# Kernel optimization log

Hardware: AMD Instinct MI355X
Metric: run time of the kernel (lower is better)

Reference implementation:

```python
import jax, jax.numpy as jnp
import numpy as np

HEAD_SIZE = 64
N_EMBED = 1024
THETA = 10000.0


def _rope_cos_sin(T, dim):
    # freqs = 1/theta^(2i/dim), i in [0, dim//2)
    freqs = 1.0 / (THETA ** (jnp.arange(0, dim, 2, dtype=jnp.float32) / dim))  # (dim//2,)
    angles = jnp.arange(T, dtype=jnp.float32)[:, None] * freqs[None, :]        # (T, dim//2)
    return jnp.cos(angles), jnp.sin(angles)


def _apply_rope(q, cos, sin):
    # q: (B, T, hs); interpret consecutive pairs as complex (even=real, odd=imag)
    B, T, hs = q.shape
    qr = q.reshape(B, T, hs // 2, 2)
    ev, od = qr[..., 0], qr[..., 1]
    out_ev = ev * cos - od * sin
    out_od = ev * sin + od * cos
    return jnp.stack([out_ev, out_od], axis=-1).reshape(B, T, hs)


def setup_inputs() -> dict:
    key = jax.random.key(0)
    ks = jax.random.split(key, 7)
    B, T = 4, 2048
    s = 1.0 / np.sqrt(N_EMBED)
    return {
        "x": jax.random.normal(ks[0], (B, T, N_EMBED), dtype=jnp.float32),
        "mask": jnp.ones((B, T), dtype=jnp.int32),
        "Wq": jax.random.uniform(ks[1], (N_EMBED, HEAD_SIZE), jnp.float32, -s, s),
        "bq": jax.random.uniform(ks[2], (HEAD_SIZE,), jnp.float32, -s, s),
        "Wk": jax.random.uniform(ks[3], (N_EMBED, HEAD_SIZE), jnp.float32, -s, s),
        "bk": jax.random.uniform(ks[4], (HEAD_SIZE,), jnp.float32, -s, s),
        "Wv": jax.random.uniform(ks[5], (N_EMBED, HEAD_SIZE), jnp.float32, -s, s),
        "bv": jax.random.uniform(ks[6], (HEAD_SIZE,), jnp.float32, -s, s),
    }


def reference(x, mask, Wq, bq, Wk, bk, Wv, bv):
    B, T, C = x.shape
    Q = x @ Wq + bq  # (B, T, hs)
    K = x @ Wk + bk
    V = x @ Wv + bv

    cos, sin = _rope_cos_sin(T, HEAD_SIZE)
    Q = _apply_rope(Q, cos, sin)
    K = _apply_rope(K, cos, sin)

    causal = jnp.triu(jnp.ones((T, T), dtype=bool), k=1)[None, :, :]  # (1, T, T)
    pad = (mask == 0)[:, :, None]                                     # (B, T, 1) masks rows
    attn_mask = causal | pad                                          # (B, T, T)

    scores = jnp.einsum('btd,bsd->bts', Q, K) * (C ** -0.5)
    scores = jnp.where(attn_mask, -jnp.inf, scores)
    attn = jax.nn.softmax(scores, axis=-1)
    # dropout in eval mode: identity
    return jnp.einsum('bts,bsd->btd', attn, V)
```

## Files before the change

kernel.cpp:

```cpp
#include <hip/hip_runtime.h>
#include <math.h>


typedef __attribute__((ext_vector_type(8))) short short8v;
typedef __attribute__((ext_vector_type(4))) float f32x4;

__device__ __forceinline__ unsigned short f2bf(float f){
  unsigned int u = __float_as_uint(f);
  u += 0x7fffu + ((u >> 16) & 1u);
  return (unsigned short)(u >> 16);
}
__device__ __forceinline__ float bf2f(unsigned short h){
  return __uint_as_float(((unsigned int)h) << 16);
}
__device__ __forceinline__ f32x4 mfma16(short8v a, short8v b, f32x4 c){
  return __builtin_amdgcn_mfma_f32_16x16x32_bf16(a, b, c, 0, 0, 0);
}


__global__ __launch_bounds__(256) void prep_k(
    const float* __restrict__ Wq, const float* __restrict__ Wk, const float* __restrict__ Wv,
    unsigned short* __restrict__ WThi, unsigned short* __restrict__ WTlo,
    float2* __restrict__ rope)
{
  const int tid = blockIdx.x * 256 + threadIdx.x;
  #pragma unroll
  for (int it = 0; it < 3; ++it){
    const int idx = tid + 65536 * it;
    const int k = idx / 192;
    const int n = idx - k * 192;
    const float v = (n < 64) ? Wq[k*64 + n] : (n < 128 ? Wk[k*64 + n - 64] : Wv[k*64 + n - 128]);
    const unsigned short hi = f2bf(v);
    WThi[n*1024 + k] = hi;
    WTlo[n*1024 + k] = f2bf(v - bf2f(hi));
  }
  const int p = tid & 31, tt = tid >> 5;
  const float freq = exp2f((float)p * -0.4152410118609203f);
  float s, c;
  sincosf((float)tt * freq, &s, &c);
  rope[tid] = make_float2(c, s);
}

__global__ __launch_bounds__(256) void qkv_k(
    const float* __restrict__ x,
    const unsigned short* __restrict__ WThi, const unsigned short* __restrict__ WTlo,
    const float* __restrict__ bq, const float* __restrict__ bk, const float* __restrict__ bv,
    const float2* __restrict__ rope,
    unsigned short* __restrict__ Qhi, unsigned short* __restrict__ Qlo,
    unsigned short* __restrict__ Khi, unsigned short* __restrict__ Klo,
    unsigned short* __restrict__ VThi, unsigned short* __restrict__ VTlo)
{
  __shared__ __align__(16) unsigned short XAh[32][72], XAl[32][72];
  __shared__ __align__(16) unsigned short WTh[192][72], WTl[192][72];

  const int t = threadIdx.x;
  const int w = t >> 6, l = t & 63;
  const int h = w & 1, nh = w >> 1;
  const int g = l >> 4, c16 = l & 15;
  const int m0 = blockIdx.x * 32;

  f32x4 acc[6];
  #pragma unroll
  for (int nt = 0; nt < 6; ++nt) acc[nt] = (f32x4){0.f, 0.f, 0.f, 0.f};

  const int xr = t >> 3, xc = (t & 7) * 8;

  for (int k0 = 0; k0 < 1024; k0 += 64){
    __syncthreads();
    {
      const float* xp = &x[(m0 + xr) * 1024 + k0 + xc];
      const float4 a = *(const float4*)xp;
      const float4 b4 = *(const float4*)(xp + 4);
      const float f[8] = {a.x, a.y, a.z, a.w, b4.x, b4.y, b4.z, b4.w};
      union { short8v v; unsigned short u[8]; } hh, ll;
      #pragma unroll
      for (int j = 0; j < 8; ++j){
        hh.u[j] = f2bf(f[j]);
        ll.u[j] = f2bf(f[j] - bf2f(hh.u[j]));
      }
      *(short8v*)&XAh[xr][xc] = hh.v;
      *(short8v*)&XAl[xr][xc] = ll.v;
    }
    #pragma unroll
    for (int a = 0; a < 6; ++a){
      const int ch = t + 256 * a;
      const int wn = ch >> 3, wk = (ch & 7) * 8;
      *(short8v*)&WTh[wn][wk] = *(const short8v*)&WThi[wn*1024 + k0 + wk];
      *(short8v*)&WTl[wn][wk] = *(const short8v*)&WTlo[wn*1024 + k0 + wk];
    }
    __syncthreads();
    #pragma unroll
    for (int ks = 0; ks < 2; ++ks){
      const short8v ah = *(const short8v*)&XAh[16*h + c16][ks*32 + g*8];
      const short8v al2 = *(const short8v*)&XAl[16*h + c16][ks*32 + g*8];
      #pragma unroll
      for (int nt = 0; nt < 6; ++nt){
        const int wr = 96*nh + 16*nt + c16;
        const short8v bh = *(const short8v*)&WTh[wr][ks*32 + g*8];
        const short8v bl = *(const short8v*)&WTl[wr][ks*32 + g*8];
        acc[nt] = mfma16(ah, bh, acc[nt]);
        acc[nt] = mfma16(ah, bl, acc[nt]);
        acc[nt] = mfma16(al2, bh, acc[nt]);
      }
    }
  }

  #pragma unroll
  for (int nt = 0; nt < 6; ++nt){
    const int c = 96*nh + 16*nt + c16;
    const int m = c >> 6, cm = c & 63;
    const float* bptr = (m == 0) ? bq : (m == 1 ? bk : bv);
    const float bias = bptr[cm];
    #pragma unroll
    for (int i = 0; i < 4; ++i){
      const int gr = m0 + 16*h + 4*g + i;
      float v = acc[nt][i] + bias;
      const float other = __shfl_xor(v, 1);
      if (m < 2){
        const float2 cs = rope[(gr & 2047) * 32 + (cm >> 1)];
        v = (c & 1) ? fmaf(v, cs.x,  other * cs.y)
                    : fmaf(v, cs.x, -other * cs.y);
      }
      const unsigned short hi = f2bf(v);
      const unsigned short lo = f2bf(v - bf2f(hi));
      if (m == 0){ Qhi[gr*64 + cm] = hi; Qlo[gr*64 + cm] = lo; }
      else if (m == 1){ Khi[gr*64 + cm] = hi; Klo[gr*64 + cm] = lo; }
      else {
        const size_t a2 = ((size_t)(gr >> 11) * 64 + cm) * 2048 + (gr & 2047);
        VThi[a2] = hi; VTlo[a2] = lo;
      }
    }
  }
}

__global__ __launch_bounds__(256) void attn_k(
    const unsigned short* __restrict__ Qhi, const unsigned short* __restrict__ Qlo,
    const unsigned short* __restrict__ Khi, const unsigned short* __restrict__ Klo,
    const unsigned short* __restrict__ VThi, const unsigned short* __restrict__ VTlo,
    float* __restrict__ out)
{
  __shared__ __align__(16) unsigned short Kh[64][72], Kl[64][72];
  __shared__ __align__(16) unsigned short Vh[64][72], Vl[64][72];
  __shared__ __align__(16) unsigned short Ph[4][16][40], Pl[4][16][40];
  __shared__ float Om[2][16][68];
  __shared__ float Ml[2][16][2];

  const int t = threadIdx.x;
  const int w = t >> 6, l = t & 63;
  const int h = w & 1, kh = w >> 1;
  const int g = l >> 4, c16 = l & 15;
  const int b = blockIdx.y;
  const int q0 = (63 - (int)blockIdx.x) * 32;
  const size_t bT = (size_t)b * 2048;

  short8v qh[2], ql2[2];
  {
    const size_t qoff = (bT + q0 + 16*h + c16) * 64 + g*8;
    qh[0]  = *(const short8v*)&Qhi[qoff];
    qh[1]  = *(const short8v*)&Qhi[qoff + 32];
    ql2[0] = *(const short8v*)&Qlo[qoff];
    ql2[1] = *(const short8v*)&Qlo[qoff + 32];
  }

  f32x4 acc[4];
  #pragma unroll
  for (int nt = 0; nt < 4; ++nt) acc[nt] = (f32x4){0.f, 0.f, 0.f, 0.f};
  float m_run[4], l_run[4];
  #pragma unroll
  for (int i = 0; i < 4; ++i){ m_run[i] = -INFINITY; l_run[i] = 0.f; }

  const int sr = t >> 2, sc = (t & 3) * 16;
  const int nk = q0 / 64 + 1;

  for (int kt = 0; kt < nk; ++kt){
    const int k0 = kt * 64;
    __syncthreads();
    {
      const size_t koff = (bT + k0 + sr) * 64 + sc;
      *(short8v*)&Kh[sr][sc]     = *(const short8v*)&Khi[koff];
      *(short8v*)&Kh[sr][sc + 8] = *(const short8v*)&Khi[koff + 8];
      *(short8v*)&Kl[sr][sc]     = *(const short8v*)&Klo[koff];
      *(short8v*)&Kl[sr][sc + 8] = *(const short8v*)&Klo[koff + 8];
      const size_t voff = ((size_t)b * 64 + sr) * 2048 + k0 + sc;
      *(short8v*)&Vh[sr][sc]     = *(const short8v*)&VThi[voff];
      *(short8v*)&Vh[sr][sc + 8] = *(const short8v*)&VThi[voff + 8];
      *(short8v*)&Vl[sr][sc]     = *(const short8v*)&VTlo[voff];
      *(short8v*)&Vl[sr][sc + 8] = *(const short8v*)&VTlo[voff + 8];
    }
    __syncthreads();

    f32x4 s[2];
    #pragma unroll
    for (int t2 = 0; t2 < 2; ++t2){
      const int krow = 32*kh + 16*t2 + c16;
      const short8v bh0 = *(const short8v*)&Kh[krow][g*8];
      const short8v bl0 = *(const short8v*)&Kl[krow][g*8];
      const short8v bh1 = *(const short8v*)&Kh[krow][32 + g*8];
      const short8v bl1 = *(const short8v*)&Kl[krow][32 + g*8];
      f32x4 z = (f32x4){0.f, 0.f, 0.f, 0.f};
      z = mfma16(qh[0], bh0, z);
      z = mfma16(qh[0], bl0, z);
      z = mfma16(ql2[0], bh0, z);
      z = mfma16(qh[1], bh1, z);
      z = mfma16(qh[1], bl1, z);
      z = mfma16(ql2[1], bh1, z);
      s[t2] = z;
    }

    float sv[2][4];
    #pragma unroll
    for (int t2 = 0; t2 < 2; ++t2)
      #pragma unroll
      for (int i = 0; i < 4; ++i){
        float v = s[t2][i] * 0.03125f;
        if (kt == nk - 1){
          const int keyg = k0 + 32*kh + 16*t2 + c16;
          const int qg = q0 + 16*h + 4*g + i;
          if (keyg > qg) v = -INFINITY;
        }
        sv[t2][i] = v;
      }

    float al[4];
    #pragma unroll
    for (int i = 0; i < 4; ++i){
      float pm = fmaxf(sv[0][i], sv[1][i]);
      pm = fmaxf(pm, __shfl_xor(pm, 1));
      pm = fmaxf(pm, __shfl_xor(pm, 2));
      pm = fmaxf(pm, __shfl_xor(pm, 4));
      pm = fmaxf(pm, __shfl_xor(pm, 8));
      const float mnew = fmaxf(m_run[i], pm);
      const float msafe = fmaxf(mnew, -1e30f);
      al[i] = expf(m_run[i] - msafe);
      const float p0 = expf(sv[0][i] - msafe);
      const float p1 = expf(sv[1][i] - msafe);
      float ps = p0 + p1;
      ps += __shfl_xor(ps, 1);
      ps += __shfl_xor(ps, 2);
      ps += __shfl_xor(ps, 4);
      ps += __shfl_xor(ps, 8);
      l_run[i] = l_run[i] * al[i] + ps;
      m_run[i] = mnew;
      const unsigned short h0 = f2bf(p0);
      Ph[w][4*g + i][c16] = h0;
      Pl[w][4*g + i][c16] = f2bf(p0 - bf2f(h0));
      const unsigned short h1 = f2bf(p1);
      Ph[w][4*g + i][16 + c16] = h1;
      Pl[w][4*g + i][16 + c16] = f2bf(p1 - bf2f(h1));
    }

    #pragma unroll
    for (int nt = 0; nt < 4; ++nt)
      #pragma unroll
      for (int i = 0; i < 4; ++i) acc[nt][i] *= al[i];

    const short8v pah = *(const short8v*)&Ph[w][c16][g*8];
    const short8v pal = *(const short8v*)&Pl[w][c16][g*8];
    #pragma unroll
    for (int nt = 0; nt < 4; ++nt){
      const short8v vbh = *(const short8v*)&Vh[16*nt + c16][32*kh + g*8];
      const short8v vbl = *(const short8v*)&Vl[16*nt + c16][32*kh + g*8];
      acc[nt] = mfma16(pah, vbh, acc[nt]);
      acc[nt] = mfma16(pah, vbl, acc[nt]);
      acc[nt] = mfma16(pal, vbh, acc[nt]);
    }
  }

  if (kh == 1){
    #pragma unroll
    for (int nt = 0; nt < 4; ++nt)
      #pragma unroll
      for (int i = 0; i < 4; ++i)
        Om[h][4*g + i][16*nt + c16] = acc[nt][i];
    if (c16 == 0){
      #pragma unroll
      for (int i = 0; i < 4; ++i){
        Ml[h][4*g + i][0] = m_run[i];
        Ml[h][4*g + i][1] = l_run[i];
      }
    }
  }
  __syncthreads();
  if (kh == 0){
    float e0[4], e1[4], linv[4];
    #pragma unroll
    for (int i = 0; i < 4; ++i){
      const float mo  = Ml[h][4*g + i][0];
      const float lo2 = Ml[h][4*g + i][1];
      const float mm = fmaxf(m_run[i], mo);
      e0[i] = expf(m_run[i] - mm);
      e1[i] = (mo == -INFINITY) ? 0.f : expf(mo - mm);
      linv[i] = 1.f / (l_run[i] * e0[i] + lo2 * e1[i]);
    }
    #pragma unroll
    for (int nt = 0; nt < 4; ++nt)
      #pragma unroll
      for (int i = 0; i < 4; ++i){
        const float v = (acc[nt][i] * e0[i] + Om[h][4*g + i][16*nt + c16] * e1[i]) * linv[i];
        out[(bT + q0 + 16*h + 4*g + i) * 64 + 16*nt + c16] = v;
      }
  }
}

extern "C" void kernel_launch(void* const* d_in, const int* in_sizes, int n_in,
                              void* d_out, int out_size, void* d_ws, size_t ws_size,
                              hipStream_t stream) {
  (void)in_sizes; (void)n_in; (void)out_size; (void)ws_size;
  const float* x    = (const float*)d_in[0];
  const float* Wq   = (const float*)d_in[2];
  const float* bq   = (const float*)d_in[3];
  const float* Wk   = (const float*)d_in[4];
  const float* bk   = (const float*)d_in[5];
  const float* Wv   = (const float*)d_in[6];
  const float* bv   = (const float*)d_in[7];
  float* out = (float*)d_out;

  const size_t NROW = 8192;
  unsigned short* Qhi  = (unsigned short*)d_ws;
  unsigned short* Qlo  = Qhi  + NROW * 64;
  unsigned short* Khi  = Qlo  + NROW * 64;
  unsigned short* Klo  = Khi  + NROW * 64;
  unsigned short* VThi = Klo  + NROW * 64;
  unsigned short* VTlo = VThi + NROW * 64;
  unsigned short* WThi = VTlo + NROW * 64;
  unsigned short* WTlo = WThi + 192 * 1024;
  float2*         rope = (float2*)(WTlo + 192 * 1024);

  prep_k<<<dim3(256), dim3(256), 0, stream>>>(Wq, Wk, Wv, WThi, WTlo, rope);
  qkv_k<<<dim3(256), dim3(256), 0, stream>>>(x, WThi, WTlo, bq, bk, bv, rope,
                                             Qhi, Qlo, Khi, Klo, VThi, VTlo);
  attn_k<<<dim3(64, 4), dim3(256), 0, stream>>>(Qhi, Qlo, Khi, Klo, VThi, VTlo, out);
}
```

Baseline: 180.7 us.

## Drop split-bf16 Q/K/V in attention, use 512 threads and register prefetch

Q, K, V and P are now stored as a single bf16 value instead of a hi/lo split, so the attention MFMAs go from three per product to one. Both kernels move to 512 threads (8 waves), and attention splits each key tile across four wave groups whose partial softmax states are merged at the end. K/V for the next tile are prefetched into registers before the current tile is computed. Dropping the lo parts lowers accuracy, and the P·V MFMA zero-pads half its K dimension.

```diff
diff --git a/kernel.cpp b/kernel.cpp
--- a/kernel.cpp
+++ b/kernel.cpp
@@ -3,6 +3,7 @@
 
 
 typedef __attribute__((ext_vector_type(8))) short short8v;
+typedef __attribute__((ext_vector_type(4))) short short4v;
 typedef __attribute__((ext_vector_type(4))) float f32x4;
 
 __device__ __forceinline__ unsigned short f2bf(float f){
@@ -41,14 +42,13 @@
   rope[tid] = make_float2(c, s);
 }
 
-__global__ __launch_bounds__(256) void qkv_k(
+__global__ __launch_bounds__(512) void qkv_k(
     const float* __restrict__ x,
     const unsigned short* __restrict__ WThi, const unsigned short* __restrict__ WTlo,
     const float* __restrict__ bq, const float* __restrict__ bk, const float* __restrict__ bv,
     const float2* __restrict__ rope,
-    unsigned short* __restrict__ Qhi, unsigned short* __restrict__ Qlo,
-    unsigned short* __restrict__ Khi, unsigned short* __restrict__ Klo,
-    unsigned short* __restrict__ VThi, unsigned short* __restrict__ VTlo)
+    unsigned short* __restrict__ Qb, unsigned short* __restrict__ Kb,
+    unsigned short* __restrict__ VT)
 {
   __shared__ __align__(16) unsigned short XAh[32][72], XAl[32][72];
   __shared__ __align__(16) unsigned short WTh[192][72], WTl[192][72];
@@ -59,31 +59,29 @@
   const int g = l >> 4, c16 = l & 15;
   const int m0 = blockIdx.x * 32;
 
-  f32x4 acc[6];
-  #pragma unroll
-  for (int nt = 0; nt < 6; ++nt) acc[nt] = (f32x4){0.f, 0.f, 0.f, 0.f};
-
-  const int xr = t >> 3, xc = (t & 7) * 8;
+  f32x4 acc[3];
+  #pragma unroll
+  for (int nt = 0; nt < 3; ++nt) acc[nt] = (f32x4){0.f, 0.f, 0.f, 0.f};
+
+  const int xr = t >> 4, xc = (t & 15) * 4;
 
   for (int k0 = 0; k0 < 1024; k0 += 64){
     __syncthreads();
     {
-      const float* xp = &x[(m0 + xr) * 1024 + k0 + xc];
-      const float4 a = *(const float4*)xp;
-      const float4 b4 = *(const float4*)(xp + 4);
-      const float f[8] = {a.x, a.y, a.z, a.w, b4.x, b4.y, b4.z, b4.w};
-      union { short8v v; unsigned short u[8]; } hh, ll;
-      #pragma unroll
-      for (int j = 0; j < 8; ++j){
+      const float4 a4 = *(const float4*)&x[(m0 + xr) * 1024 + k0 + xc];
+      const float f[4] = {a4.x, a4.y, a4.z, a4.w};
+      union { short4v v; unsigned short u[4]; } hh, ll;
+      #pragma unroll
+      for (int j = 0; j < 4; ++j){
         hh.u[j] = f2bf(f[j]);
         ll.u[j] = f2bf(f[j] - bf2f(hh.u[j]));
       }
-      *(short8v*)&XAh[xr][xc] = hh.v;
-      *(short8v*)&XAl[xr][xc] = ll.v;
-    }
-    #pragma unroll
-    for (int a = 0; a < 6; ++a){
-      const int ch = t + 256 * a;
+      *(short4v*)&XAh[xr][xc] = hh.v;
+      *(short4v*)&XAl[xr][xc] = ll.v;
+    }
+    #pragma unroll
+    for (int a = 0; a < 3; ++a){
+      const int ch = t + 512 * a;
       const int wn = ch >> 3, wk = (ch & 7) * 8;
       *(short8v*)&WTh[wn][wk] = *(const short8v*)&WThi[wn*1024 + k0 + wk];
       *(short8v*)&WTl[wn][wk] = *(const short8v*)&WTlo[wn*1024 + k0 + wk];
@@ -91,11 +89,11 @@
     __syncthreads();
     #pragma unroll
     for (int ks = 0; ks < 2; ++ks){
-      const short8v ah = *(const short8v*)&XAh[16*h + c16][ks*32 + g*8];
+      const short8v ah  = *(const short8v*)&XAh[16*h + c16][ks*32 + g*8];
       const short8v al2 = *(const short8v*)&XAl[16*h + c16][ks*32 + g*8];
       #pragma unroll
-      for (int nt = 0; nt < 6; ++nt){
-        const int wr = 96*nh + 16*nt + c16;
+      for (int nt = 0; nt < 3; ++nt){
+        const int wr = 48*nh + 16*nt + c16;
         const short8v bh = *(const short8v*)&WTh[wr][ks*32 + g*8];
         const short8v bl = *(const short8v*)&WTl[wr][ks*32 + g*8];
         acc[nt] = mfma16(ah, bh, acc[nt]);
@@ -106,8 +104,8 @@
   }
 
   #pragma unroll
-  for (int nt = 0; nt < 6; ++nt){
-    const int c = 96*nh + 16*nt + c16;
+  for (int nt = 0; nt < 3; ++nt){
+    const int c = 48*nh + 16*nt + c16;
     const int m = c >> 6, cm = c & 63;
     const float* bptr = (m == 0) ? bq : (m == 1 ? bk : bv);
     const float bias = bptr[cm];
@@ -121,29 +119,22 @@
         v = (c & 1) ? fmaf(v, cs.x,  other * cs.y)
                     : fmaf(v, cs.x, -other * cs.y);
       }
-      const unsigned short hi = f2bf(v);
-      const unsigned short lo = f2bf(v - bf2f(hi));
-      if (m == 0){ Qhi[gr*64 + cm] = hi; Qlo[gr*64 + cm] = lo; }
-      else if (m == 1){ Khi[gr*64 + cm] = hi; Klo[gr*64 + cm] = lo; }
-      else {
-        const size_t a2 = ((size_t)(gr >> 11) * 64 + cm) * 2048 + (gr & 2047);
-        VThi[a2] = hi; VTlo[a2] = lo;
-      }
-    }
-  }
-}
-
-__global__ __launch_bounds__(256) void attn_k(
-    const unsigned short* __restrict__ Qhi, const unsigned short* __restrict__ Qlo,
-    const unsigned short* __restrict__ Khi, const unsigned short* __restrict__ Klo,
-    const unsigned short* __restrict__ VThi, const unsigned short* __restrict__ VTlo,
-    float* __restrict__ out)
+      if (m == 0)      Qb[gr*64 + cm] = f2bf(v);
+      else if (m == 1) Kb[gr*64 + cm] = f2bf(v);
+      else             VT[((size_t)(gr >> 11) * 64 + cm) * 2048 + (gr & 2047)] = f2bf(v);
+    }
+  }
+}
+
+__global__ __launch_bounds__(512) void attn_k(
+    const unsigned short* __restrict__ Qb, const unsigned short* __restrict__ Kb,
+    const unsigned short* __restrict__ VT, float* __restrict__ out)
 {
-  __shared__ __align__(16) unsigned short Kh[64][72], Kl[64][72];
-  __shared__ __align__(16) unsigned short Vh[64][72], Vl[64][72];
-  __shared__ __align__(16) unsigned short Ph[4][16][40], Pl[4][16][40];
-  __shared__ float Om[2][16][68];
-  __shared__ float Ml[2][16][2];
+  __shared__ __align__(16) unsigned short Kh[64][72];
+  __shared__ __align__(16) unsigned short Vh[64][72];
+  __shared__ __align__(16) unsigned short Ph[8][16][24];
+  __shared__ float Om[2][3][16][68];
+  __shared__ float Ml[2][3][16][2];
 
   const int t = threadIdx.x;
   const int w = t >> 6, l = t & 63;
@@ -153,13 +144,11 @@
   const int q0 = (63 - (int)blockIdx.x) * 32;
   const size_t bT = (size_t)b * 2048;
 
-  short8v qh[2], ql2[2];
+  short8v qh[2];
   {
     const size_t qoff = (bT + q0 + 16*h + c16) * 64 + g*8;
-    qh[0]  = *(const short8v*)&Qhi[qoff];
-    qh[1]  = *(const short8v*)&Qhi[qoff + 32];
-    ql2[0] = *(const short8v*)&Qlo[qoff];
-    ql2[1] = *(const short8v*)&Qlo[qoff + 32];
+    qh[0] = *(const short8v*)&Qb[qoff];
+    qh[1] = *(const short8v*)&Qb[qoff + 32];
   }
 
   f32x4 acc[4];
@@ -169,62 +158,48 @@
   #pragma unroll
   for (int i = 0; i < 4; ++i){ m_run[i] = -INFINITY; l_run[i] = 0.f; }
 
-  const int sr = t >> 2, sc = (t & 3) * 16;
+  const int sr = t >> 3, sc = (t & 7) * 8;
   const int nk = q0 / 64 + 1;
 
+  short8v kreg = *(const short8v*)&Kb[(bT + sr) * 64 + sc];
+  short8v vreg = *(const short8v*)&VT[((size_t)b * 64 + sr) * 2048 + sc];
+
   for (int kt = 0; kt < nk; ++kt){
+    __syncthreads();
+    *(short8v*)&Kh[sr][sc] = kreg;
+    *(short8v*)&Vh[sr][sc] = vreg;
+    if (kt + 1 < nk){
+      const int k1 = (kt + 1) * 64;
+      kreg = *(const short8v*)&Kb[(bT + k1 + sr) * 64 + sc];
+      vreg = *(const short8v*)&VT[((size_t)b * 64 + sr) * 2048 + k1 + sc];
+    }
+    __syncthreads();
+
     const int k0 = kt * 64;
-    __syncthreads();
+    f32x4 z = (f32x4){0.f, 0.f, 0.f, 0.f};
     {
-      const size_t koff = (bT + k0 + sr) * 64 + sc;
-      *(short8v*)&Kh[sr][sc]     = *(const short8v*)&Khi[koff];
-      *(short8v*)&Kh[sr][sc + 8] = *(const short8v*)&Khi[koff + 8];
-      *(short8v*)&Kl[sr][sc]     = *(const short8v*)&Klo[koff];
-      *(short8v*)&Kl[sr][sc + 8] = *(const short8v*)&Klo[koff + 8];
-      const size_t voff = ((size_t)b * 64 + sr) * 2048 + k0 + sc;
-      *(short8v*)&Vh[sr][sc]     = *(const short8v*)&VThi[voff];
-      *(short8v*)&Vh[sr][sc + 8] = *(const short8v*)&VThi[voff + 8];
-      *(short8v*)&Vl[sr][sc]     = *(const short8v*)&VTlo[voff];
-      *(short8v*)&Vl[sr][sc + 8] = *(const short8v*)&VTlo[voff + 8];
-    }
-    __syncthreads();
-
-    f32x4 s[2];
-    #pragma unroll
-    for (int t2 = 0; t2 < 2; ++t2){
-      const int krow = 32*kh + 16*t2 + c16;
-      const short8v bh0 = *(const short8v*)&Kh[krow][g*8];
-      const short8v bl0 = *(const short8v*)&Kl[krow][g*8];
-      const short8v bh1 = *(const short8v*)&Kh[krow][32 + g*8];
-      const short8v bl1 = *(const short8v*)&Kl[krow][32 + g*8];
-      f32x4 z = (f32x4){0.f, 0.f, 0.f, 0.f};
-      z = mfma16(qh[0], bh0, z);
-      z = mfma16(qh[0], bl0, z);
-      z = mfma16(ql2[0], bh0, z);
-      z = mfma16(qh[1], bh1, z);
-      z = mfma16(qh[1], bl1, z);
-      z = mfma16(ql2[1], bh1, z);
-      s[t2] = z;
-    }
-
-    float sv[2][4];
-    #pragma unroll
-    for (int t2 = 0; t2 < 2; ++t2)
-      #pragma unroll
-      for (int i = 0; i < 4; ++i){
-        float v = s[t2][i] * 0.03125f;
-        if (kt == nk - 1){
-          const int keyg = k0 + 32*kh + 16*t2 + c16;
-          const int qg = q0 + 16*h + 4*g + i;
-          if (keyg > qg) v = -INFINITY;
-        }
-        sv[t2][i] = v;
-      }
+      const short8v kb0 = *(const short8v*)&Kh[16*kh + c16][g*8];
+      const short8v kb1 = *(const short8v*)&Kh[16*kh + c16][32 + g*8];
+      z = mfma16(qh[0], kb0, z);
+      z = mfma16(qh[1], kb1, z);
+    }
+
+    float sv[4];
+    #pragma unroll
+    for (int i = 0; i < 4; ++i){
+      float v = z[i] * 0.03125f;
+      if (kt == nk - 1){
+        const int keyg = k0 + 16*kh + c16;
+        const int qg = q0 + 16*h + 4*g + i;
+        if (keyg > qg) v = -INFINITY;
+      }
+      sv[i] = v;
+    }
 
     float al[4];
     #pragma unroll
     for (int i = 0; i < 4; ++i){
-      float pm = fmaxf(sv[0][i], sv[1][i]);
+      float pm = sv[i];
       pm = fmaxf(pm, __shfl_xor(pm, 1));
       pm = fmaxf(pm, __shfl_xor(pm, 2));
       pm = fmaxf(pm, __shfl_xor(pm, 4));
@@ -232,21 +207,15 @@
       const float mnew = fmaxf(m_run[i], pm);
       const float msafe = fmaxf(mnew, -1e30f);
       al[i] = expf(m_run[i] - msafe);
-      const float p0 = expf(sv[0][i] - msafe);
-      const float p1 = expf(sv[1][i] - msafe);
-      float ps = p0 + p1;
+      const float p0 = expf(sv[i] - msafe);
+      float ps = p0;
       ps += __shfl_xor(ps, 1);
       ps += __shfl_xor(ps, 2);
       ps += __shfl_xor(ps, 4);
       ps += __shfl_xor(ps, 8);
       l_run[i] = l_run[i] * al[i] + ps;
       m_run[i] = mnew;
-      const unsigned short h0 = f2bf(p0);
-      Ph[w][4*g + i][c16] = h0;
-      Pl[w][4*g + i][c16] = f2bf(p0 - bf2f(h0));
-      const unsigned short h1 = f2bf(p1);
-      Ph[w][4*g + i][16 + c16] = h1;
-      Pl[w][4*g + i][16 + c16] = f2bf(p1 - bf2f(h1));
+      Ph[w][4*g + i][c16] = f2bf(p0);
     }
 
     #pragma unroll
@@ -254,50 +223,62 @@
       #pragma unroll
       for (int i = 0; i < 4; ++i) acc[nt][i] *= al[i];
 
-    const short8v pah = *(const short8v*)&Ph[w][c16][g*8];
-    const short8v pal = *(const short8v*)&Pl[w][c16][g*8];
+    short8v pa;
+    if (g < 2) pa = *(const short8v*)&Ph[w][c16][g*8];
+    else       pa = (short8v){0,0,0,0,0,0,0,0};
+    const int kcol = 16*kh + 8*(g & 1);
     #pragma unroll
     for (int nt = 0; nt < 4; ++nt){
-      const short8v vbh = *(const short8v*)&Vh[16*nt + c16][32*kh + g*8];
-      const short8v vbl = *(const short8v*)&Vl[16*nt + c16][32*kh + g*8];
-      acc[nt] = mfma16(pah, vbh, acc[nt]);
-      acc[nt] = mfma16(pah, vbl, acc[nt]);
-      acc[nt] = mfma16(pal, vbh, acc[nt]);
-    }
-  }
-
-  if (kh == 1){
+      const short8v vb = *(const short8v*)&Vh[16*nt + c16][kcol];
+      acc[nt] = mfma16(pa, vb, acc[nt]);
+    }
+  }
+
+  if (kh > 0){
     #pragma unroll
     for (int nt = 0; nt < 4; ++nt)
       #pragma unroll
       for (int i = 0; i < 4; ++i)
-        Om[h][4*g + i][16*nt + c16] = acc[nt][i];
+        Om[h][kh-1][4*g + i][16*nt + c16] = acc[nt][i];
     if (c16 == 0){
       #pragma unroll
       for (int i = 0; i < 4; ++i){
-        Ml[h][4*g + i][0] = m_run[i];
-        Ml[h][4*g + i][1] = l_run[i];
+        Ml[h][kh-1][4*g + i][0] = m_run[i];
+        Ml[h][kh-1][4*g + i][1] = l_run[i];
       }
     }
   }
   __syncthreads();
   if (kh == 0){
-    float e0[4], e1[4], linv[4];
+    float es[4], e[3][4], linv[4];
     #pragma unroll
     for (int i = 0; i < 4; ++i){
-      const float mo  = Ml[h][4*g + i][0];
-      const float lo2 = Ml[h][4*g + i][1];
-      const float mm = fmaxf(m_run[i], mo);
-      e0[i] = expf(m_run[i] - mm);
-      e1[i] = (mo == -INFINITY) ? 0.f : expf(mo - mm);
-      linv[i] = 1.f / (l_run[i] * e0[i] + lo2 * e1[i]);
+      float mo[3], lo[3];
+      float mm = m_run[i];
+      #pragma unroll
+      for (int j = 0; j < 3; ++j){
+        mo[j] = Ml[h][j][4*g + i][0];
+        lo[j] = Ml[h][j][4*g + i][1];
+        mm = fmaxf(mm, mo[j]);
+      }
+      es[i] = expf(m_run[i] - mm);
+      float lt = l_run[i] * es[i];
+      #pragma unroll
+      for (int j = 0; j < 3; ++j){
+        e[j][i] = (mo[j] == -INFINITY) ? 0.f : expf(mo[j] - mm);
+        lt += lo[j] * e[j][i];
+      }
+      linv[i] = 1.f / lt;
     }
     #pragma unroll
     for (int nt = 0; nt < 4; ++nt)
       #pragma unroll
       for (int i = 0; i < 4; ++i){
-        const float v = (acc[nt][i] * e0[i] + Om[h][4*g + i][16*nt + c16] * e1[i]) * linv[i];
-        out[(bT + q0 + 16*h + 4*g + i) * 64 + 16*nt + c16] = v;
+        float v = acc[nt][i] * es[i];
+        #pragma unroll
+        for (int j = 0; j < 3; ++j)
+          v += Om[h][j][4*g + i][16*nt + c16] * e[j][i];
+        out[(bT + q0 + 16*h + 4*g + i) * 64 + 16*nt + c16] = v * linv[i];
       }
   }
 }
@@ -316,18 +297,15 @@
   float* out = (float*)d_out;
 
   const size_t NROW = 8192;
-  unsigned short* Qhi  = (unsigned short*)d_ws;
-  unsigned short* Qlo  = Qhi  + NROW * 64;
-  unsigned short* Khi  = Qlo  + NROW * 64;
-  unsigned short* Klo  = Khi  + NROW * 64;
-  unsigned short* VThi = Klo  + NROW * 64;
-  unsigned short* VTlo = VThi + NROW * 64;
-  unsigned short* WThi = VTlo + NROW * 64;
+  unsigned short* Qb   = (unsigned short*)d_ws;
+  unsigned short* Kb   = Qb  + NROW * 64;
+  unsigned short* VT   = Kb  + NROW * 64;
+  unsigned short* WThi = VT  + NROW * 64;
   unsigned short* WTlo = WThi + 192 * 1024;
   float2*         rope = (float2*)(WTlo + 192 * 1024);
 
   prep_k<<<dim3(256), dim3(256), 0, stream>>>(Wq, Wk, Wv, WThi, WTlo, rope);
-  qkv_k<<<dim3(256), dim3(256), 0, stream>>>(x, WThi, WTlo, bq, bk, bv, rope,
-                                             Qhi, Qlo, Khi, Klo, VThi, VTlo);
-  attn_k<<<dim3(64, 4), dim3(256), 0, stream>>>(Qhi, Qlo, Khi, Klo, VThi, VTlo, out);
-}
+  qkv_k<<<dim3(256), dim3(512), 0, stream>>>(x, WThi, WTlo, bq, bk, bv, rope,
+                                             Qb, Kb, VT);
+  attn_k<<<dim3(64, 4), dim3(512), 0, stream>>>(Qb, Kb, VT, out);
+}
```

New measurement: 162.7 us. -10.0%, faster.
